# Kernel optimization log

Hardware: AMD Instinct MI355X
Metric: run time of the kernel (lower is better)

## Reference

```python
import jax, jax.numpy as jnp
import numpy as np
from functools import partial

HIDDEN = 16  # LSTM hidden_size
PROJ = 2     # LSTM proj_size
N_IN = 2     # LSTM input_size (= n_inputs)


def _lstm_cell(c, h, x, W_ih, W_hh, b_ih, b_hh, W_hr):
    # PyTorch gate order: input, forget, cell(g), output
    gates = x @ W_ih.T + h @ W_hh.T + (b_ih + b_hh)  # [B, 4*HIDDEN]
    i, f, g, o = jnp.split(gates, 4, axis=-1)
    c_new = jax.nn.sigmoid(f) * c + jax.nn.sigmoid(i) * jnp.tanh(g)
    h_new = (jax.nn.sigmoid(o) * jnp.tanh(c_new)) @ W_hr.T  # projected hidden [B, PROJ]
    return c_new, h_new


def setup_inputs() -> dict:
    key = jax.random.key(0)
    ks = jax.random.split(key, 6)
    B, T = 4096, 2048
    s = 1.0 / np.sqrt(HIDDEN)  # PyTorch LSTM init scale
    u_train = jax.random.normal(ks[0], (B, T, N_IN + PROJ), dtype=jnp.float32)
    W_ih = jax.random.uniform(ks[1], (4 * HIDDEN, N_IN), jnp.float32, -s, s)
    W_hh = jax.random.uniform(ks[2], (4 * HIDDEN, PROJ), jnp.float32, -s, s)
    b_ih = jax.random.uniform(ks[3], (4 * HIDDEN,), jnp.float32, -s, s)
    b_hh = jax.random.uniform(ks[4], (4 * HIDDEN,), jnp.float32, -s, s)
    W_hr = jax.random.uniform(ks[5], (PROJ, HIDDEN), jnp.float32, -s, s)
    return {"u_train": u_train, "W_ih": W_ih, "W_hh": W_hh, "b_ih": b_ih,
            "b_hh": b_hh, "W_hr": W_hr, "n_context": 1024}


def reference(u_train, W_ih, W_hh, b_ih, b_hh, W_hr, n_context):
    u = u_train[:, :, :N_IN]       # LSTM inputs [B, T, 2]
    y = u_train[:, :, N_IN:]       # injected hidden states [B, T, 2]
    B = u.shape[0]
    cell = partial(_lstm_cell, W_ih=W_ih, W_hh=W_hh, b_ih=b_ih, b_hh=b_hh, W_hr=W_hr)
    c0 = jnp.zeros((B, HIDDEN), u.dtype)

    # Phase 1 (estimate_state): hidden state is overwritten by y each step; only c is carried.
    def step_est(c, xy):
        x, h_inj = xy
        c_new, h_new = cell(c, h_inj, x)
        return c_new, h_new

    xs1 = (u[:, :n_context].swapaxes(0, 1), y[:, :n_context].swapaxes(0, 1))  # time-major
    c_fin, hs1 = jax.lax.scan(step_est, c0, xs1)   # hs1: [n_context, B, PROJ]
    hn = hs1[-1]

    # Phase 2 (predict_state): standard LSTM recurrence from (hn, c_fin).
    def step_pred(carry, x):
        c, h = carry
        c_new, h_new = cell(c, h, x)
        return (c_new, h_new), h_new

    _, hs2 = jax.lax.scan(step_pred, (c_fin, hn), u[:, n_context:].swapaxes(0, 1))

    y_sim = jnp.concatenate([hs1, hs2], axis=0).swapaxes(0, 1)  # [B, T, PROJ]
    return y_sim
```

## Files before the change

kernel.cpp:

```cpp
#include <hip/hip_runtime.h>

#define T_STEPS 2048
#define SEQS_PER_BLOCK 16

__device__ __forceinline__ float fast_rcp(float x) { return __builtin_amdgcn_rcpf(x); }
__device__ __forceinline__ float fast_exp2(float x) { return __builtin_amdgcn_exp2f(x); }

#define LOG2E   1.4426950408889634f
#define LOG2E2  2.8853900817779268f

__device__ __forceinline__ float fsigmoid(float x) {
    return fast_rcp(1.0f + fast_exp2(x * -LOG2E));
}
__device__ __forceinline__ float ftanh_fast(float x) {
    return fmaf(-2.0f, fast_rcp(1.0f + fast_exp2(x * LOG2E2)), 1.0f);
}

template<int CTRL>
__device__ __forceinline__ float dpp_ror_add(float v) {
    int t = __builtin_amdgcn_update_dpp(0, __float_as_int(v), CTRL, 0xF, 0xF, true);
    return v + __int_as_float(t);
}
__device__ __forceinline__ float row16_allreduce(float v) {
    v = dpp_ror_add<0x121>(v);
    v = dpp_ror_add<0x122>(v);
    v = dpp_ror_add<0x124>(v);
    v = dpp_ror_add<0x128>(v);
    return v;
}

extern "C" __global__ __launch_bounds__(256) void lstm_seq_kernel(
    const float* __restrict__ u,
    const float* __restrict__ Wih,
    const float* __restrict__ Whh,
    const float* __restrict__ bih,
    const float* __restrict__ bhh,
    const float* __restrict__ Whr,
    const int* __restrict__ ncp,
    float* __restrict__ out,
    int B)
{
    const int lane = threadIdx.x & 15;
    const int grp  = threadIdx.x >> 4;
    const int seq  = blockIdx.x * SEQS_PER_BLOCK + grp;
    if (seq >= B) return;

    const int nc = *ncp;

    const int ri = lane, rf = lane + 16, rg = lane + 32, ro = lane + 48;
    const float2 wih_i = ((const float2*)Wih)[ri];
    const float2 wih_f = ((const float2*)Wih)[rf];
    const float2 wih_g = ((const float2*)Wih)[rg];
    const float2 wih_o = ((const float2*)Wih)[ro];
    const float2 whh_i = ((const float2*)Whh)[ri];
    const float2 whh_f = ((const float2*)Whh)[rf];
    const float2 whh_g = ((const float2*)Whh)[rg];
    const float2 whh_o = ((const float2*)Whh)[ro];
    const float bi = bih[ri] + bhh[ri];
    const float bf = bih[rf] + bhh[rf];
    const float bg = bih[rg] + bhh[rg];
    const float bo = bih[ro] + bhh[ro];
    const float whr0 = Whr[lane];
    const float whr1 = Whr[16 + lane];

    const float*  up  = u + (size_t)seq * T_STEPS * 4;
    const float4* upv = (const float4*)up;
    float*        op  = out + (size_t)seq * T_STEPS * 2;

    float c  = 0.0f;
    float h0 = 0.0f, h1 = 0.0f;
    float bh0 = 0.0f, bh1 = 0.0f;

    auto step = [&](const float4 cur, int t, bool injected) {
        const float x0 = cur.x, x1 = cur.y;
        const float hh0 = injected ? cur.z : h0;
        const float hh1 = injected ? cur.w : h1;

        float pi = fmaf(hh0, whh_i.x, fmaf(hh1, whh_i.y, fmaf(x0, wih_i.x, fmaf(x1, wih_i.y, bi))));
        float pf = fmaf(hh0, whh_f.x, fmaf(hh1, whh_f.y, fmaf(x0, wih_f.x, fmaf(x1, wih_f.y, bf))));
        float pg = fmaf(hh0, whh_g.x, fmaf(hh1, whh_g.y, fmaf(x0, wih_g.x, fmaf(x1, wih_g.y, bg))));
        float po = fmaf(hh0, whh_o.x, fmaf(hh1, whh_o.y, fmaf(x0, wih_o.x, fmaf(x1, wih_o.y, bo))));

        const float si = fsigmoid(pi);
        const float sf = fsigmoid(pf);
        const float so = fsigmoid(po);
        const float tg = ftanh_fast(pg);

        c = fmaf(sf, c, si * tg);
        const float m = so * ftanh_fast(c);

        h0 = row16_allreduce(m * whr0);
        h1 = row16_allreduce(m * whr1);

        const int s = t & 15;
        bh0 = (s == lane) ? h0 : bh0;
        bh1 = (s == lane) ? h1 : bh1;
        if (s == 15) {
            ((float2*)(op + 2 * (t - 15)))[lane] = make_float2(bh0, bh1);
        }
    };

    float4 q0 = upv[0], q1 = upv[1], q2 = upv[2], q3 = upv[3];
    int tb = 0;

    #pragma unroll 2
    for (; tb < nc; tb += 4) {
        const int nb = tb + 4;
        float4 n0 = upv[nb];
        float4 n1 = upv[nb + 1];
        float4 n2 = upv[nb + 2];
        float4 n3 = upv[nb + 3];
        step(q0, tb,     true);
        step(q1, tb + 1, true);
        step(q2, tb + 2, true);
        step(q3, tb + 3, true);
        q0 = n0; q1 = n1; q2 = n2; q3 = n3;
    }

    #pragma unroll 2
    for (; tb < T_STEPS; tb += 4) {
        const int nb = (tb + 4 < T_STEPS) ? tb + 4 : T_STEPS - 4;
        float4 n0 = upv[nb];
        float4 n1 = upv[nb + 1];
        float4 n2 = upv[nb + 2];
        float4 n3 = upv[nb + 3];
        step(q0, tb,     false);
        step(q1, tb + 1, false);
        step(q2, tb + 2, false);
        step(q3, tb + 3, false);
        q0 = n0; q1 = n1; q2 = n2; q3 = n3;
    }
}

extern "C" void kernel_launch(void* const* d_in, const int* in_sizes, int n_in,
                              void* d_out, int out_size, void* d_ws, size_t ws_size,
                              hipStream_t stream) {
    const float* u   = (const float*)d_in[0];
    const float* Wih = (const float*)d_in[1];
    const float* Whh = (const float*)d_in[2];
    const float* bih = (const float*)d_in[3];
    const float* bhh = (const float*)d_in[4];
    const float* Whr = (const float*)d_in[5];
    const int*   ncp = (const int*)d_in[6];
    float* out = (float*)d_out;

    const int B = in_sizes[0] / (T_STEPS * 4);
    const int blocks = (B + SEQS_PER_BLOCK - 1) / SEQS_PER_BLOCK;

    hipLaunchKernelGGL(lstm_seq_kernel, dim3(blocks), dim3(256), 0, stream,
                       u, Wih, Whh, bih, bhh, Whr, ncp, out, B);
}
```

Before: 631.5 us.

## Split LSTM into separate estimate and predict phase kernels via workspace

```diff
diff --git a/kernel.cpp b/kernel.cpp
--- a/kernel.cpp
+++ b/kernel.cpp
@@ -29,16 +29,36 @@
     return v;
 }
 
-extern "C" __global__ __launch_bounds__(256) void lstm_seq_kernel(
-    const float* __restrict__ u,
-    const float* __restrict__ Wih,
-    const float* __restrict__ Whh,
-    const float* __restrict__ bih,
-    const float* __restrict__ bhh,
-    const float* __restrict__ Whr,
-    const int* __restrict__ ncp,
-    float* __restrict__ out,
-    int B)
+struct LaneW {
+    float2 wih_i, wih_f, wih_g, wih_o;
+    float2 whh_i, whh_f, whh_g, whh_o;
+    float  bi, bf, bg, bo;
+    float  whr0, whr1;
+};
+
+__device__ __forceinline__ LaneW load_lane_weights(
+    const float* __restrict__ Wih, const float* __restrict__ Whh,
+    const float* __restrict__ bih, const float* __restrict__ bhh,
+    const float* __restrict__ Whr, int lane)
+{
+    LaneW w;
+    const int ri = lane, rf = lane + 16, rg = lane + 32, ro = lane + 48;
+    w.wih_i = ((const float2*)Wih)[ri];  w.wih_f = ((const float2*)Wih)[rf];
+    w.wih_g = ((const float2*)Wih)[rg];  w.wih_o = ((const float2*)Wih)[ro];
+    w.whh_i = ((const float2*)Whh)[ri];  w.whh_f = ((const float2*)Whh)[rf];
+    w.whh_g = ((const float2*)Whh)[rg];  w.whh_o = ((const float2*)Whh)[ro];
+    w.bi = bih[ri] + bhh[ri];  w.bf = bih[rf] + bhh[rf];
+    w.bg = bih[rg] + bhh[rg];  w.bo = bih[ro] + bhh[ro];
+    w.whr0 = Whr[lane];  w.whr1 = Whr[16 + lane];
+    return w;
+}
+
+extern "C" __global__ __launch_bounds__(256) void lstm_phase1_kernel(
+    const float* __restrict__ u, const float* __restrict__ Wih,
+    const float* __restrict__ Whh, const float* __restrict__ bih,
+    const float* __restrict__ bhh, const float* __restrict__ Whr,
+    const int* __restrict__ ncp, float* __restrict__ out,
+    float* __restrict__ ws_c, float* __restrict__ ws_h, int B)
 {
     const int lane = threadIdx.x & 15;
     const int grp  = threadIdx.x >> 4;
@@ -47,39 +67,23 @@
 
     const int nc = *ncp;
 
-    const int ri = lane, rf = lane + 16, rg = lane + 32, ro = lane + 48;
-    const float2 wih_i = ((const float2*)Wih)[ri];
-    const float2 wih_f = ((const float2*)Wih)[rf];
-    const float2 wih_g = ((const float2*)Wih)[rg];
-    const float2 wih_o = ((const float2*)Wih)[ro];
-    const float2 whh_i = ((const float2*)Whh)[ri];
-    const float2 whh_f = ((const float2*)Whh)[rf];
-    const float2 whh_g = ((const float2*)Whh)[rg];
-    const float2 whh_o = ((const float2*)Whh)[ro];
-    const float bi = bih[ri] + bhh[ri];
-    const float bf = bih[rf] + bhh[rf];
-    const float bg = bih[rg] + bhh[rg];
-    const float bo = bih[ro] + bhh[ro];
-    const float whr0 = Whr[lane];
-    const float whr1 = Whr[16 + lane];
-
-    const float*  up  = u + (size_t)seq * T_STEPS * 4;
-    const float4* upv = (const float4*)up;
+    const LaneW w = load_lane_weights(Wih, Whh, bih, bhh, Whr, lane);
+
+    const float4* upv = (const float4*)(u + (size_t)seq * T_STEPS * 4);
     float*        op  = out + (size_t)seq * T_STEPS * 2;
 
-    float c  = 0.0f;
+    float c = 0.0f;
     float h0 = 0.0f, h1 = 0.0f;
     float bh0 = 0.0f, bh1 = 0.0f;
 
-    auto step = [&](const float4 cur, int t, bool injected) {
+    auto step = [&](const float4 cur, int t) {
         const float x0 = cur.x, x1 = cur.y;
-        const float hh0 = injected ? cur.z : h0;
-        const float hh1 = injected ? cur.w : h1;
-
-        float pi = fmaf(hh0, whh_i.x, fmaf(hh1, whh_i.y, fmaf(x0, wih_i.x, fmaf(x1, wih_i.y, bi))));
-        float pf = fmaf(hh0, whh_f.x, fmaf(hh1, whh_f.y, fmaf(x0, wih_f.x, fmaf(x1, wih_f.y, bf))));
-        float pg = fmaf(hh0, whh_g.x, fmaf(hh1, whh_g.y, fmaf(x0, wih_g.x, fmaf(x1, wih_g.y, bg))));
-        float po = fmaf(hh0, whh_o.x, fmaf(hh1, whh_o.y, fmaf(x0, wih_o.x, fmaf(x1, wih_o.y, bo))));
+        const float hh0 = cur.z, hh1 = cur.w;
+
+        float pi = fmaf(hh0, w.whh_i.x, fmaf(hh1, w.whh_i.y, fmaf(x0, w.wih_i.x, fmaf(x1, w.wih_i.y, w.bi))));
+        float pf = fmaf(hh0, w.whh_f.x, fmaf(hh1, w.whh_f.y, fmaf(x0, w.wih_f.x, fmaf(x1, w.wih_f.y, w.bf))));
+        float pg = fmaf(hh0, w.whh_g.x, fmaf(hh1, w.whh_g.y, fmaf(x0, w.wih_g.x, fmaf(x1, w.wih_g.y, w.bg))));
+        float po = fmaf(hh0, w.whh_o.x, fmaf(hh1, w.whh_o.y, fmaf(x0, w.wih_o.x, fmaf(x1, w.wih_o.y, w.bo))));
 
         const float si = fsigmoid(pi);
         const float sf = fsigmoid(pf);
@@ -89,8 +93,8 @@
         c = fmaf(sf, c, si * tg);
         const float m = so * ftanh_fast(c);
 
-        h0 = row16_allreduce(m * whr0);
-        h1 = row16_allreduce(m * whr1);
+        h0 = row16_allreduce(m * w.whr0);
+        h1 = row16_allreduce(m * w.whr1);
 
         const int s = t & 15;
         bh0 = (s == lane) ? h0 : bh0;
@@ -101,33 +105,90 @@
     };
 
     float4 q0 = upv[0], q1 = upv[1], q2 = upv[2], q3 = upv[3];
-    int tb = 0;
-
     #pragma unroll 2
-    for (; tb < nc; tb += 4) {
+    for (int tb = 0; tb < nc; tb += 4) {
         const int nb = tb + 4;
         float4 n0 = upv[nb];
         float4 n1 = upv[nb + 1];
         float4 n2 = upv[nb + 2];
         float4 n3 = upv[nb + 3];
-        step(q0, tb,     true);
-        step(q1, tb + 1, true);
-        step(q2, tb + 2, true);
-        step(q3, tb + 3, true);
+        step(q0, tb);
+        step(q1, tb + 1);
+        step(q2, tb + 2);
+        step(q3, tb + 3);
         q0 = n0; q1 = n1; q2 = n2; q3 = n3;
     }
 
+    ws_c[(size_t)seq * 16 + lane] = c;
+    if (lane == 0) {
+        ((float2*)ws_h)[seq] = make_float2(h0, h1);
+    }
+}
+
+extern "C" __global__ __launch_bounds__(256) void lstm_phase2_kernel(
+    const float* __restrict__ u, const float* __restrict__ Wih,
+    const float* __restrict__ Whh, const float* __restrict__ bih,
+    const float* __restrict__ bhh, const float* __restrict__ Whr,
+    const int* __restrict__ ncp, float* __restrict__ out,
+    const float* __restrict__ ws_c, const float* __restrict__ ws_h, int B)
+{
+    const int lane = threadIdx.x & 15;
+    const int grp  = threadIdx.x >> 4;
+    const int seq  = blockIdx.x * SEQS_PER_BLOCK + grp;
+    if (seq >= B) return;
+
+    const int nc = *ncp;
+
+    const LaneW w = load_lane_weights(Wih, Whh, bih, bhh, Whr, lane);
+
+    const float4* upv = (const float4*)(u + (size_t)seq * T_STEPS * 4);
+    float*        op  = out + (size_t)seq * T_STEPS * 2;
+
+    float c = ws_c[(size_t)seq * 16 + lane];
+    const float2 hh = ((const float2*)ws_h)[seq];
+    float h0 = hh.x, h1 = hh.y;
+    float bh0 = 0.0f, bh1 = 0.0f;
+
+    auto step = [&](const float4 cur, int t) {
+        const float x0 = cur.x, x1 = cur.y;
+        const float hh0 = h0, hh1 = h1;
+
+        float pi = fmaf(hh0, w.whh_i.x, fmaf(hh1, w.whh_i.y, fmaf(x0, w.wih_i.x, fmaf(x1, w.wih_i.y, w.bi))));
+        float pf = fmaf(hh0, w.whh_f.x, fmaf(hh1, w.whh_f.y, fmaf(x0, w.wih_f.x, fmaf(x1, w.wih_f.y, w.bf))));
+        float pg = fmaf(hh0, w.whh_g.x, fmaf(hh1, w.whh_g.y, fmaf(x0, w.wih_g.x, fmaf(x1, w.wih_g.y, w.bg))));
+        float po = fmaf(hh0, w.whh_o.x, fmaf(hh1, w.whh_o.y, fmaf(x0, w.wih_o.x, fmaf(x1, w.wih_o.y, w.bo))));
+
+        const float si = fsigmoid(pi);
+        const float sf = fsigmoid(pf);
+        const float so = fsigmoid(po);
+        const float tg = ftanh_fast(pg);
+
+        c = fmaf(sf, c, si * tg);
+        const float m = so * ftanh_fast(c);
+
+        h0 = row16_allreduce(m * w.whr0);
+        h1 = row16_allreduce(m * w.whr1);
+
+        const int s = t & 15;
+        bh0 = (s == lane) ? h0 : bh0;
+        bh1 = (s == lane) ? h1 : bh1;
+        if (s == 15) {
+            ((float2*)(op + 2 * (t - 15)))[lane] = make_float2(bh0, bh1);
+        }
+    };
+
+    float4 q0 = upv[nc], q1 = upv[nc + 1], q2 = upv[nc + 2], q3 = upv[nc + 3];
     #pragma unroll 2
-    for (; tb < T_STEPS; tb += 4) {
+    for (int tb = nc; tb < T_STEPS; tb += 4) {
         const int nb = (tb + 4 < T_STEPS) ? tb + 4 : T_STEPS - 4;
         float4 n0 = upv[nb];
         float4 n1 = upv[nb + 1];
         float4 n2 = upv[nb + 2];
         float4 n3 = upv[nb + 3];
-        step(q0, tb,     false);
-        step(q1, tb + 1, false);
-        step(q2, tb + 2, false);
-        step(q3, tb + 3, false);
+        step(q0, tb);
+        step(q1, tb + 1);
+        step(q2, tb + 2);
+        step(q3, tb + 3);
         q0 = n0; q1 = n1; q2 = n2; q3 = n3;
     }
 }
@@ -147,6 +208,11 @@
     const int B = in_sizes[0] / (T_STEPS * 4);
     const int blocks = (B + SEQS_PER_BLOCK - 1) / SEQS_PER_BLOCK;
 
-    hipLaunchKernelGGL(lstm_seq_kernel, dim3(blocks), dim3(256), 0, stream,
-                       u, Wih, Whh, bih, bhh, Whr, ncp, out, B);
-}
+    float* ws_c = (float*)d_ws;
+    float* ws_h = ws_c + (size_t)B * 16;
+
+    hipLaunchKernelGGL(lstm_phase1_kernel, dim3(blocks), dim3(256), 0, stream,
+                       u, Wih, Whh, bih, bhh, Whr, ncp, out, ws_c, ws_h, B);
+    hipLaunchKernelGGL(lstm_phase2_kernel, dim3(blocks), dim3(256), 0, stream,
+                       u, Wih, Whh, bih, bhh, Whr, ncp, out, ws_c, ws_h, B);
+}
```

New measurement: 532.7 us. 15.6% less time.
